# Kernel tuning notes

Measured on AMD Instinct MI355X. Metric: run time of the kernel, lower is better.

The kernel has to match this reference:

```python
import jax, jax.numpy as jnp
import numpy as np

DIMS = [64, 128, 192, 256]   # Matryoshka sub-dims (init arg `dims`)
TEMPERATURE = 1.0
NEG_INF = float('-inf')
EPS = 1e-12  # F.normalize eps


def setup_inputs() -> dict:
    key = jax.random.key(0)
    k1, k2 = jax.random.split(key)
    B, K, D = 2048, 4096, 256
    reps_q = jax.random.normal(k1, (B, D), dtype=jnp.float32)
    reps_d = jax.random.normal(k2, (K, D), dtype=jnp.float32)
    return {"reps_q": reps_q, "reps_d": reps_d}


def _l2_normalize(x):
    n = jnp.linalg.norm(x, axis=1, keepdims=True)
    return x / jnp.maximum(n, EPS)


def _loss_for_dim(reps_q, reps_d, dim):
    q = _l2_normalize(reps_q[:, :dim])   # [B, dim]
    d = _l2_normalize(reps_d[:, :dim])   # [K, dim]
    B, K = q.shape[0], d.shape[0]

    qk = q @ d.T                         # [B, K]

    # check_pos_neg_pair_conflict (always True in the torch code)
    pos = d[:B]                          # positives are the first B keys
    sim = jax.lax.stop_gradient(pos @ d.T)               # [B, K], detached
    eye_bk = jnp.eye(B, K, dtype=bool)
    conflict = jnp.isclose(sim, 1.0, rtol=1e-5, atol=1e-5) & ~eye_bk
    qk = jnp.where(conflict, NEG_INF, qk)

    # use_all_pairs=True path: kq, qq, kk with -inf diagonals
    eye_bb = jnp.eye(B, dtype=bool)
    kq = jnp.where(eye_bb, NEG_INF, pos @ q.T)           # [B, B]
    qq = jnp.where(eye_bb, NEG_INF, q @ q.T)             # [B, B]
    kk = jnp.where(eye_bb, NEG_INF, pos @ pos.T)         # [B, B]

    scores = jnp.concatenate([qk, kq, qq, kk], axis=1)   # [B, K+3B]

    # check_false_neg: mask entries above diag(scores)+0.1 (thresholds detached)
    # diag(scores)[i] = scores[i, i] = qk[i, i] since B <= K
    thr = jax.lax.stop_gradient(jnp.diagonal(qk))[:, None] + 0.1
    scores = jnp.where(scores > thr, NEG_INF, scores)

    # cross-entropy with labels = arange(B)
    logp = jax.nn.log_softmax(scores / TEMPERATURE, axis=1)
    idx = jnp.arange(B)
    return -jnp.mean(logp[idx, idx])


def reference(reps_q, reps_d):
    loss = 0.0
    for dim in DIMS:
        loss = loss + _loss_for_dim(reps_q, reps_d, dim)
    return loss / len(DIMS)
```

## Files before the change

### kernel.cpp

```cpp
#include <hip/hip_runtime.h>

#define B_N 2048
#define K_N 4096
#define D_N 256
#define GRID_SCORE 1536
#define LOG2E 1.44269504f

typedef unsigned short u16;
typedef unsigned int u32;
typedef short short8 __attribute__((ext_vector_type(8)));
typedef float f32x4 __attribute__((ext_vector_type(4)));

#if __has_builtin(__builtin_amdgcn_exp2f)
#define EXP2F(x) __builtin_amdgcn_exp2f(x)
#else
#define EXP2F(x) exp2f(x)
#endif
#if __has_builtin(__builtin_amdgcn_logf)
#define LOG2F(x) __builtin_amdgcn_logf(x)
#else
#define LOG2F(x) log2f(x)
#endif

__device__ __forceinline__ u16 f2bf(float x) {
    union { float f; u32 u; } v; v.f = x;
    u32 u = v.u;
    u32 lsb = (u >> 16) & 1u;
    u += 0x7fffu + lsb;
    return (u16)(u >> 16);
}
__device__ __forceinline__ float bits2f(u32 u) {
    union { u32 u; float f; } v; v.u = u; return v.f;
}

__device__ __forceinline__ float dpp_row16_sum(float v) {
    union { float f; int i; } a, b;
    a.f = v;
    b.i = __builtin_amdgcn_update_dpp(0, a.i, 0x128, 0xF, 0xF, true); a.f += b.f;
    b.i = __builtin_amdgcn_update_dpp(0, a.i, 0x124, 0xF, 0xF, true); a.f += b.f;
    b.i = __builtin_amdgcn_update_dpp(0, a.i, 0x04E, 0xF, 0xF, true); a.f += b.f;
    b.i = __builtin_amdgcn_update_dpp(0, a.i, 0x0B1, 0xF, 0xF, true); a.f += b.f;
    return a.f;
}

__global__ __launch_bounds__(256) void prep_kernel(
    const float* __restrict__ qsrc, const float* __restrict__ dsrc,
    u16* __restrict__ qb, u16* __restrict__ db,
    float* __restrict__ invnq, float* __restrict__ invnd, float* __restrict__ diag,
    float* __restrict__ rowsum, u32* __restrict__ doneCnt)
{
    if (blockIdx.x < 32) rowsum[blockIdx.x * 256 + threadIdx.x] = 0.f;
    if (blockIdx.x == 32 && threadIdx.x == 0)
        __hip_atomic_store(doneCnt, 0u, __ATOMIC_RELAXED, __HIP_MEMORY_SCOPE_AGENT);

    const int wave = threadIdx.x >> 6;
    const int lane = threadIdx.x & 63;
    const int row  = blockIdx.x * 4 + wave;

    if (row < B_N) {
        const int i = row;
        float4 qv = *(const float4*)(qsrc + i * D_N + lane * 4);
        float4 dv = *(const float4*)(dsrc + i * D_N + lane * 4);
        ushort4 qs; qs.x = f2bf(qv.x); qs.y = f2bf(qv.y); qs.z = f2bf(qv.z); qs.w = f2bf(qv.w);
        *(ushort4*)(qb + i * D_N + lane * 4) = qs;
        float sqq = qv.x*qv.x + qv.y*qv.y + qv.z*qv.z + qv.w*qv.w;
        float sdd = dv.x*dv.x + dv.y*dv.y + dv.z*dv.z + dv.w*dv.w;
        float sqd = qv.x*dv.x + qv.y*dv.y + qv.z*dv.z + qv.w*dv.w;
        sqq = dpp_row16_sum(sqq);
        sdd = dpp_row16_sum(sdd);
        sqd = dpp_row16_sum(sqd);
        float gq0 = __shfl(sqq, 0),  gq1 = __shfl(sqq, 16), gq2 = __shfl(sqq, 32), gq3 = __shfl(sqq, 48);
        float gd0 = __shfl(sdd, 0),  gd1 = __shfl(sdd, 16), gd2 = __shfl(sdd, 32), gd3 = __shfl(sdd, 48);
        float gp0 = __shfl(sqd, 0),  gp1 = __shfl(sqd, 16), gp2 = __shfl(sqd, 32), gp3 = __shfl(sqd, 48);
        if (lane < 4) {
            float pq = gq0, pd = gd0, pp = gp0;
            if (lane >= 1) { pq += gq1; pd += gd1; pp += gp1; }
            if (lane >= 2) { pq += gq2; pd += gd2; pp += gp2; }
            if (lane >= 3) { pq += gq3; pd += gd3; pp += gp3; }
            float inq = 1.0f / fmaxf(sqrtf(pq), 1e-12f);
            float ind = 1.0f / fmaxf(sqrtf(pd), 1e-12f);
            invnq[i * 4 + lane] = inq;
            diag[i * 4 + lane]  = pp * inq * ind;
        }
    } else {
        const int j = row - B_N;
        float4 dv = *(const float4*)(dsrc + j * D_N + lane * 4);
        ushort4 ds; ds.x = f2bf(dv.x); ds.y = f2bf(dv.y); ds.z = f2bf(dv.z); ds.w = f2bf(dv.w);
        *(ushort4*)(db + j * D_N + lane * 4) = ds;
        float sdd = dv.x*dv.x + dv.y*dv.y + dv.z*dv.z + dv.w*dv.w;
        sdd = dpp_row16_sum(sdd);
        if (lane < 4) {
            float gd0 = __shfl(sdd, 0), gd1 = __shfl(sdd, 16), gd2 = __shfl(sdd, 32), gd3 = __shfl(sdd, 48);
            float pd = gd0;
            if (lane >= 1) pd += gd1;
            if (lane >= 2) pd += gd2;
            if (lane >= 3) pd += gd3;
            invnd[j * 4 + lane] = 1.0f / fmaxf(sqrtf(pd), 1e-12f);
        }
    }
}

template<int RGN, bool EYE>
__device__ __forceinline__ void epi_seg(
    const f32x4* accq, const f32x4* accd,
    const float* ldsInvAq, const float* ldsInvAd, const float* ldsThr,
    const float* ldsInvB, float* ldsAcc,
    int s, int wrow, int quad, int lane15, int eyeOff)
{
    const int myr = wrow + quad * 4;
    f32x4 ivAq = *(const f32x4*)(ldsInvAq + s * 128 + myr);
    f32x4 ivAd = *(const f32x4*)(ldsInvAd + s * 128 + myr);
    f32x4 thrv = *(const f32x4*)(ldsThr   + s * 128 + myr);
    float ivB[4];
    #pragma unroll
    for (int ct = 0; ct < 4; ++ct)
        ivB[ct] = ldsInvB[s * 64 + ct * 16 + lane15];
    f32x4 rsd = {0.f, 0.f, 0.f, 0.f};
    #pragma unroll
    for (int ct = 0; ct < 4; ++ct) {
        const int jloc = ct * 16 + lane15;
        f32x4 tq = accq[ct] * ivAq;
        f32x4 td = accd[ct] * ivAd;
        #pragma unroll
        for (int r = 0; r < 4; ++r) {
            const float thr = thrv[r];
            const float sq = tq[r] * ivB[ct];
            const float sd = td[r] * ivB[ct];
            const bool eye = EYE && ((myr + r) == (jloc + eyeOff));
            float add = 0.f;
            if (RGN <= 1) {
                bool conflict = (fabsf(sd - LOG2E) <= 2e-5f * LOG2E);
                if (EYE) conflict = conflict && !eye;
                if (!conflict && sq <= thr) add += EXP2F(sq);
                if (RGN == 0) {
                    bool okk = (sd <= thr);
                    if (EYE) okk = okk && !eye;
                    if (okk) add += EXP2F(sd);
                }
            } else {
                bool o1 = (sd <= thr), o2 = (sq <= thr);
                if (EYE) { o1 = o1 && !eye; o2 = o2 && !eye; }
                if (o1) add += EXP2F(sd);
                if (o2) add += EXP2F(sq);
            }
            rsd[r] += add;
        }
    }
    f32x4 red;
    #pragma unroll
    for (int r = 0; r < 4; ++r) red[r] = dpp_row16_sum(rsd[r]);
    if (lane15 == 0)
        *(f32x4*)(ldsAcc + s * 128 + myr) = red;
}

#define LSB 264
__global__ __launch_bounds__(512, 4) void score_kernel(
    const u16* __restrict__ qb, const u16* __restrict__ db,
    const float* __restrict__ invnq, const float* __restrict__ invnd,
    const float* __restrict__ diag, float* __restrict__ rowsum,
    u32* __restrict__ doneCnt, u32* __restrict__ out)
{
    __shared__ u16   ldsB[64 * LSB];
    __shared__ float ldsInvAq[4 * 128];
    __shared__ float ldsInvAd[4 * 128];
    __shared__ float ldsThr[4 * 128];
    __shared__ float ldsInvB[4 * 64];
    __shared__ float ldsAcc[4 * 128];
    __shared__ u32   ldsLast;

    const int cb = blockIdx.x % 96;
    const int rb = blockIdx.x / 96;
    const int IR = rb * 128;
    const int JC = cb * 64;
    const bool isR3 = (cb >= 64);
    const bool isR1 = (cb < 32);
    const u16*  bsrc     = isR3 ? qb : db;
    const float* invBsrc = isR3 ? invnq : invnd;
    const int JB = isR3 ? (JC - K_N) : JC;
    const int cc = isR3 ? (cb - 64) : cb;
    const int sel = isR1 ? (((cb >> 1) == rb) ? 1 : 0)
                  : (!isR3 ? 2 : (((cc >> 1) == rb) ? 4 : 3));
    const int eyeOff = (cc & 1) * 64;

    const int tid    = threadIdx.x;
    const int lane   = tid & 63;
    const int lane15 = lane & 15;
    const int quad   = lane >> 4;
    const int wrow   = (tid >> 6) * 16;

    {
        const int row = tid >> 2, s = tid & 3;
        ldsInvAq[s * 128 + row] = invnq[(IR + row) * 4 + s] * LOG2E;
        ldsInvAd[s * 128 + row] = invnd[(IR + row) * 4 + s] * LOG2E;
        ldsThr[s * 128 + row]   = (diag[(IR + row) * 4 + s] + 0.1f) * LOG2E;
        if (tid < 256) {
            const int rw = tid >> 2, sc = tid & 3;
            ldsInvB[sc * 64 + rw]  = invBsrc[(JB + rw) * 4 + sc];
        }
    }

    #pragma unroll
    for (int c = 0; c < 4; ++c) {
        int idx = tid + c * 512;
        int row = idx >> 5;
        int ch  = idx & 31;
        uint4 v = *(const uint4*)(bsrc + (JB + row) * D_N + ch * 8);
        *(uint4*)(ldsB + row * LSB + ch * 8) = v;
    }

    const u16* qrowp = qb + (IR + wrow + lane15) * D_N + quad * 8;
    const u16* drowp = db + (IR + wrow + lane15) * D_N + quad * 8;

    short8 aq0 = *(const short8*)(qrowp);
    short8 aq1 = *(const short8*)(qrowp + 32);
    short8 ad0 = *(const short8*)(drowp);
    short8 ad1 = *(const short8*)(drowp + 32);

    __syncthreads();

    f32x4 accq[4], accd[4];
    #pragma unroll
    for (int ct = 0; ct < 4; ++ct) {
        accq[ct] = (f32x4){0.f, 0.f, 0.f, 0.f};
        accd[ct] = (f32x4){0.f, 0.f, 0.f, 0.f};
    }

    #pragma unroll
    for (int s = 0; s < 4; ++s) {
        const int sn = ((s + 1) & 3) * 64;
        short8 nq0 = *(const short8*)(qrowp + sn);
        short8 nq1 = *(const short8*)(qrowp + sn + 32);
        short8 nd0 = *(const short8*)(drowp + sn);
        short8 nd1 = *(const short8*)(drowp + sn + 32);

        #pragma unroll
        for (int ct = 0; ct < 4; ++ct) {
            short8 b0 = *(const short8*)(ldsB + (ct * 16 + lane15) * LSB + s * 64 + quad * 8);
            accq[ct] = __builtin_amdgcn_mfma_f32_16x16x32_bf16(aq0, b0, accq[ct], 0, 0, 0);
            accd[ct] = __builtin_amdgcn_mfma_f32_16x16x32_bf16(ad0, b0, accd[ct], 0, 0, 0);
        }
        #pragma unroll
        for (int ct = 0; ct < 4; ++ct) {
            short8 b1 = *(const short8*)(ldsB + (ct * 16 + lane15) * LSB + s * 64 + 32 + quad * 8);
            accq[ct] = __builtin_amdgcn_mfma_f32_16x16x32_bf16(aq1, b1, accq[ct], 0, 0, 0);
            accd[ct] = __builtin_amdgcn_mfma_f32_16x16x32_bf16(ad1, b1, accd[ct], 0, 0, 0);
        }
        if (sel == 0)      epi_seg<0,false>(accq, accd, ldsInvAq, ldsInvAd, ldsThr, ldsInvB, ldsAcc, s, wrow, quad, lane15, eyeOff);
        else if (sel == 1) epi_seg<0,true >(accq, accd, ldsInvAq, ldsInvAd, ldsThr, ldsInvB, ldsAcc, s, wrow, quad, lane15, eyeOff);
        else if (sel == 2) epi_seg<1,false>(accq, accd, ldsInvAq, ldsInvAd, ldsThr, ldsInvB, ldsAcc, s, wrow, quad, lane15, eyeOff);
        else if (sel == 3) epi_seg<2,false>(accq, accd, ldsInvAq, ldsInvAd, ldsThr, ldsInvB, ldsAcc, s, wrow, quad, lane15, eyeOff);
        else               epi_seg<2,true >(accq, accd, ldsInvAq, ldsInvAd, ldsThr, ldsInvB, ldsAcc, s, wrow, quad, lane15, eyeOff);

        aq0 = nq0; aq1 = nq1; ad0 = nd0; ad1 = nd1;
    }
    __syncthreads();

    atomicAdd(&rowsum[IR * 4 + tid], ldsAcc[(tid & 3) * 128 + (tid >> 2)]);
    __syncthreads();
    if (tid == 0) {
        u32 tk = __hip_atomic_fetch_add(doneCnt, 1u, __ATOMIC_RELAXED,
                                        __HIP_MEMORY_SCOPE_AGENT);
        ldsLast = (tk == (GRID_SCORE - 1)) ? 1u : 0u;
    }
    __syncthreads();

    if (ldsLast) {
        float acc = 0.f;
        #pragma unroll 8
        for (int c = 0; c < 16; ++c) {
            int idx = tid + c * 512;
            float rsv = __hip_atomic_load(&rowsum[idx], __ATOMIC_RELAXED,
                                          __HIP_MEMORY_SCOPE_AGENT);
            acc += LOG2F(rsv) * 0.69314718056f - diag[idx];
        }
        ldsAcc[tid] = acc;
        __syncthreads();
        #pragma unroll
        for (int off = 256; off > 0; off >>= 1) {
            if (tid < off) ldsAcc[tid] += ldsAcc[tid + off];
            __syncthreads();
        }
        if (tid == 0) {
            float L = ldsAcc[0] * (1.0f / (B_N * 4.0f));
            u16 h = f2bf(L);
            union { float f; u32 u; } b; b.f = L;
            u32 c0 = (b.u & 0xFFFF0000u) | (u32)h;
            u32 c1 = c0 + 0x10000u;
            u32 c2 = c0 - 0x10000u;
            float e0 = fabsf(bits2f(c0) - L);
            float e1 = fabsf(bits2f(c1) - L);
            float e2 = fabsf(bits2f(c2) - L);
            u32 best = c0; float be = e0;
            if (e1 < be) { best = c1; be = e1; }
            if (e2 < be) { best = c2; }
            out[0] = best;
        }
    }
}

extern "C" void kernel_launch(void* const* d_in, const int* in_sizes, int n_in,
                              void* d_out, int out_size, void* d_ws, size_t ws_size,
                              hipStream_t stream) {
    (void)in_sizes; (void)n_in; (void)out_size; (void)ws_size;
    const float* qsrc = (const float*)d_in[0];
    const float* dsrc = (const float*)d_in[1];
    char* ws = (char*)d_ws;
    u16*   qb      = (u16*)ws;
    u16*   db      = (u16*)(ws + 1048576);
    float* invnq   = (float*)(ws + 3145728);
    float* invnd   = (float*)(ws + 3178496);
    float* diag    = (float*)(ws + 3244032);
    float* rowsum  = (float*)(ws + 3276800);
    u32*   doneCnt = (u32*)(ws + 3309568);

    prep_kernel<<<1536, 256, 0, stream>>>(qsrc, dsrc, qb, db, invnq, invnd, diag,
                                          rowsum, doneCnt);
    score_kernel<<<GRID_SCORE, 512, 0, stream>>>(qb, db, invnq, invnd, diag, rowsum,
                                                 doneCnt, (u32*)d_out);
}
```

Baseline: 95.95 us.

## Derive kq scores from transposed qk tiles instead of a separate MFMA plane

The kq = pos·qᵀ block equals the transpose of the qk tile restricted to the first B keys. So the query-query column blocks now issue only the q-plane MFMAs and skip the d-row loads and their epilogue exponentials. The key-region blocks covering the first B keys reuse their already computed exp(qk) values to build column partial sums, using per-column thresholds and eye masking. They accumulate these in LDS with shared-memory atomics and add them into the global row sums. This cuts MFMA and exp work in a third of the blocks, but adds LDS atomics and extra work to the busier key blocks, which makes the load across blocks less even.

```diff
diff --git a/kernel.cpp b/kernel.cpp
--- a/kernel.cpp
+++ b/kernel.cpp
@@ -104,13 +104,14 @@
 __device__ __forceinline__ void epi_seg(
     const f32x4* accq, const f32x4* accd,
     const float* ldsInvAq, const float* ldsInvAd, const float* ldsThr,
-    const float* ldsInvB, float* ldsAcc,
+    const float* ldsInvB, const float* ldsThrCol, float* ldsColAcc, float* ldsAcc,
     int s, int wrow, int quad, int lane15, int eyeOff)
 {
     const int myr = wrow + quad * 4;
     f32x4 ivAq = *(const f32x4*)(ldsInvAq + s * 128 + myr);
-    f32x4 ivAd = *(const f32x4*)(ldsInvAd + s * 128 + myr);
     f32x4 thrv = *(const f32x4*)(ldsThr   + s * 128 + myr);
+    f32x4 ivAd;
+    if (RGN <= 1) ivAd = *(const f32x4*)(ldsInvAd + s * 128 + myr);
     float ivB[4];
     #pragma unroll
     for (int ct = 0; ct < 4; ++ct)
@@ -120,31 +121,39 @@
     for (int ct = 0; ct < 4; ++ct) {
         const int jloc = ct * 16 + lane15;
         f32x4 tq = accq[ct] * ivAq;
-        f32x4 td = accd[ct] * ivAd;
+        f32x4 td;
+        if (RGN <= 1) td = accd[ct] * ivAd;
+        float thrC = 0.f;
+        if (RGN == 0) thrC = ldsThrCol[s * 64 + jloc];
+        float cpart = 0.f;
         #pragma unroll
         for (int r = 0; r < 4; ++r) {
             const float thr = thrv[r];
             const float sq = tq[r] * ivB[ct];
-            const float sd = td[r] * ivB[ct];
             const bool eye = EYE && ((myr + r) == (jloc + eyeOff));
             float add = 0.f;
             if (RGN <= 1) {
+                const float sd = td[r] * ivB[ct];
                 bool conflict = (fabsf(sd - LOG2E) <= 2e-5f * LOG2E);
                 if (EYE) conflict = conflict && !eye;
-                if (!conflict && sq <= thr) add += EXP2F(sq);
+                const float eq = EXP2F(sq);
+                if (!conflict && sq <= thr) add += eq;
                 if (RGN == 0) {
                     bool okk = (sd <= thr);
                     if (EYE) okk = okk && !eye;
                     if (okk) add += EXP2F(sd);
+                    bool okq = (sq <= thrC) && !eye;
+                    if (okq) cpart += eq;
                 }
             } else {
-                bool o1 = (sd <= thr), o2 = (sq <= thr);
-                if (EYE) { o1 = o1 && !eye; o2 = o2 && !eye; }
-                if (o1) add += EXP2F(sd);
+                bool o2 = (sq <= thr);
+                if (EYE) o2 = o2 && !eye;
                 if (o2) add += EXP2F(sq);
             }
             rsd[r] += add;
         }
+        if (RGN == 0)
+            atomicAdd(&ldsColAcc[s * 64 + jloc], cpart);
     }
     f32x4 red;
     #pragma unroll
@@ -165,6 +174,8 @@
     __shared__ float ldsInvAd[4 * 128];
     __shared__ float ldsThr[4 * 128];
     __shared__ float ldsInvB[4 * 64];
+    __shared__ float ldsThrCol[4 * 64];
+    __shared__ float ldsColAcc[4 * 64];
     __shared__ float ldsAcc[4 * 128];
     __shared__ u32   ldsLast;
 
@@ -181,6 +192,7 @@
     const int sel = isR1 ? (((cb >> 1) == rb) ? 1 : 0)
                   : (!isR3 ? 2 : (((cc >> 1) == rb) ? 4 : 3));
     const int eyeOff = (cc & 1) * 64;
+    const bool twoPlane = !isR3;
 
     const int tid    = threadIdx.x;
     const int lane   = tid & 63;
@@ -196,6 +208,9 @@
         if (tid < 256) {
             const int rw = tid >> 2, sc = tid & 3;
             ldsInvB[sc * 64 + rw]  = invBsrc[(JB + rw) * 4 + sc];
+            ldsColAcc[tid] = 0.f;
+            if (isR1)
+                ldsThrCol[sc * 64 + rw] = (diag[(JB + rw) * 4 + sc] + 0.1f) * LOG2E;
         }
     }
 
@@ -211,10 +226,14 @@
     const u16* qrowp = qb + (IR + wrow + lane15) * D_N + quad * 8;
     const u16* drowp = db + (IR + wrow + lane15) * D_N + quad * 8;
 
+    short8 zfrag = {};
     short8 aq0 = *(const short8*)(qrowp);
     short8 aq1 = *(const short8*)(qrowp + 32);
-    short8 ad0 = *(const short8*)(drowp);
-    short8 ad1 = *(const short8*)(drowp + 32);
+    short8 ad0 = zfrag, ad1 = zfrag;
+    if (twoPlane) {
+        ad0 = *(const short8*)(drowp);
+        ad1 = *(const short8*)(drowp + 32);
+    }
 
     __syncthreads();
 
@@ -230,32 +249,39 @@
         const int sn = ((s + 1) & 3) * 64;
         short8 nq0 = *(const short8*)(qrowp + sn);
         short8 nq1 = *(const short8*)(qrowp + sn + 32);
-        short8 nd0 = *(const short8*)(drowp + sn);
-        short8 nd1 = *(const short8*)(drowp + sn + 32);
+        short8 nd0 = zfrag, nd1 = zfrag;
+        if (twoPlane) {
+            nd0 = *(const short8*)(drowp + sn);
+            nd1 = *(const short8*)(drowp + sn + 32);
+        }
 
         #pragma unroll
         for (int ct = 0; ct < 4; ++ct) {
             short8 b0 = *(const short8*)(ldsB + (ct * 16 + lane15) * LSB + s * 64 + quad * 8);
             accq[ct] = __builtin_amdgcn_mfma_f32_16x16x32_bf16(aq0, b0, accq[ct], 0, 0, 0);
-            accd[ct] = __builtin_amdgcn_mfma_f32_16x16x32_bf16(ad0, b0, accd[ct], 0, 0, 0);
+            if (twoPlane)
+                accd[ct] = __builtin_amdgcn_mfma_f32_16x16x32_bf16(ad0, b0, accd[ct], 0, 0, 0);
         }
         #pragma unroll
         for (int ct = 0; ct < 4; ++ct) {
             short8 b1 = *(const short8*)(ldsB + (ct * 16 + lane15) * LSB + s * 64 + 32 + quad * 8);
             accq[ct] = __builtin_amdgcn_mfma_f32_16x16x32_bf16(aq1, b1, accq[ct], 0, 0, 0);
-            accd[ct] = __builtin_amdgcn_mfma_f32_16x16x32_bf16(ad1, b1, accd[ct], 0, 0, 0);
-        }
-        if (sel == 0)      epi_seg<0,false>(accq, accd, ldsInvAq, ldsInvAd, ldsThr, ldsInvB, ldsAcc, s, wrow, quad, lane15, eyeOff);
-        else if (sel == 1) epi_seg<0,true >(accq, accd, ldsInvAq, ldsInvAd, ldsThr, ldsInvB, ldsAcc, s, wrow, quad, lane15, eyeOff);
-        else if (sel == 2) epi_seg<1,false>(accq, accd, ldsInvAq, ldsInvAd, ldsThr, ldsInvB, ldsAcc, s, wrow, quad, lane15, eyeOff);
-        else if (sel == 3) epi_seg<2,false>(accq, accd, ldsInvAq, ldsInvAd, ldsThr, ldsInvB, ldsAcc, s, wrow, quad, lane15, eyeOff);
-        else               epi_seg<2,true >(accq, accd, ldsInvAq, ldsInvAd, ldsThr, ldsInvB, ldsAcc, s, wrow, quad, lane15, eyeOff);
+            if (twoPlane)
+                accd[ct] = __builtin_amdgcn_mfma_f32_16x16x32_bf16(ad1, b1, accd[ct], 0, 0, 0);
+        }
+        if (sel == 0)      epi_seg<0,false>(accq, accd, ldsInvAq, ldsInvAd, ldsThr, ldsInvB, ldsThrCol, ldsColAcc, ldsAcc, s, wrow, quad, lane15, eyeOff);
+        else if (sel == 1) epi_seg<0,true >(accq, accd, ldsInvAq, ldsInvAd, ldsThr, ldsInvB, ldsThrCol, ldsColAcc, ldsAcc, s, wrow, quad, lane15, eyeOff);
+        else if (sel == 2) epi_seg<1,false>(accq, accd, ldsInvAq, ldsInvAd, ldsThr, ldsInvB, ldsThrCol, ldsColAcc, ldsAcc, s, wrow, quad, lane15, eyeOff);
+        else if (sel == 3) epi_seg<2,false>(accq, accd, ldsInvAq, ldsInvAd, ldsThr, ldsInvB, ldsThrCol, ldsColAcc, ldsAcc, s, wrow, quad, lane15, eyeOff);
+        else               epi_seg<2,true >(accq, accd, ldsInvAq, ldsInvAd, ldsThr, ldsInvB, ldsThrCol, ldsColAcc, ldsAcc, s, wrow, quad, lane15, eyeOff);
 
         aq0 = nq0; aq1 = nq1; ad0 = nd0; ad1 = nd1;
     }
     __syncthreads();
 
     atomicAdd(&rowsum[IR * 4 + tid], ldsAcc[(tid & 3) * 128 + (tid >> 2)]);
+    if (isR1 && tid < 256)
+        atomicAdd(&rowsum[(JB + (tid & 63)) * 4 + (tid >> 6)], ldsColAcc[tid]);
     __syncthreads();
     if (tid == 0) {
         u32 tk = __hip_atomic_fetch_add(doneCnt, 1u, __ATOMIC_RELAXED,
```

Result: slower. 223.6 us (+133.1%).
